# Optimization experiments

Measured on AMD Instinct MI355X. Metric: run time of the kernel, lower is better.

The kernel has to match this reference:

```python
import jax, jax.numpy as jnp
import numpy as np

N = 50000        # nodes
E = 800000       # edges (avg degree 16)
F = 64           # NUM_NODE_FEATURES == NUM_FILTERS
P = 32           # allocation.NUM_PHYS (policy logits per graph)
G = 64           # graphs in batch
MAX_DEG = 10     # PyG MFConv default max_degree


def setup_inputs() -> dict:
    key = jax.random.key(0)
    ks = jax.random.split(key, 12)
    x = jax.random.normal(ks[0], (N, F), jnp.float32)
    edge_index = jax.random.randint(ks[1], (2, E), 0, N, dtype=jnp.int32)
    batch = jnp.sort(jax.random.randint(ks[2], (N,), 0, G, dtype=jnp.int32))
    s = 1.0 / np.sqrt(F)
    return {
        "x": x,
        "edge_index": edge_index,
        "batch": batch,
        # GCNConv conv_in: F -> F
        "W_in": jax.random.normal(ks[3], (F, F), jnp.float32) * s,
        "b_in": jnp.zeros((F,), jnp.float32),
        # GCNConv conv_1: F -> F
        "W1": jax.random.normal(ks[4], (F, F), jnp.float32) * s,
        "b1": jnp.zeros((F,), jnp.float32),
        # MFConv conv_val: F -> 1, per-degree weights (deg 0..MAX_DEG)
        "Wl_val": jax.random.normal(ks[5], (MAX_DEG + 1, F, 1), jnp.float32) * s,
        "bl_val": jnp.zeros((MAX_DEG + 1, 1), jnp.float32),
        "Wr_val": jax.random.normal(ks[6], (MAX_DEG + 1, F, 1), jnp.float32) * s,
        # GCNConv conv_policy: F -> P
        "W_pol": jax.random.normal(ks[7], (F, P), jnp.float32) * s,
        "b_pol": jnp.zeros((P,), jnp.float32),
    }


def gcn_conv(x, edge_index, W, b):
    # PyG GCNConv: add self-loops, symmetric normalization, linear, scatter-add.
    src, dst = edge_index[0], edge_index[1]
    loop = jnp.arange(N, dtype=src.dtype)
    src = jnp.concatenate([src, loop])
    dst = jnp.concatenate([dst, loop])
    deg = jax.ops.segment_sum(jnp.ones_like(dst, x.dtype), dst, num_segments=N)
    dinv = jnp.where(deg > 0, jax.lax.rsqrt(deg), 0.0)
    norm = dinv[src] * dinv[dst]                 # [E+N]
    h = x @ W                                    # [N, out]
    out = jax.ops.segment_sum(norm[:, None] * h[src], dst, num_segments=N)
    return out + b


def mf_conv(x, edge_index, Wl, bl, Wr):
    # PyG MFConv: sum-aggregate neighbors, per-degree linear transforms.
    src, dst = edge_index[0], edge_index[1]
    h = jax.ops.segment_sum(x[src], dst, num_segments=N)     # neighbor sum [N,F]
    deg = jax.ops.segment_sum(jnp.ones((src.shape[0],), jnp.int32), dst, num_segments=N)
    deg = jnp.clip(deg, 0, MAX_DEG)                          # [N]
    # out = lins_l[deg](h) + lins_r[deg](x)  (lins_r has no bias)
    out = (jnp.einsum("nf,nfo->no", h, Wl[deg]) + bl[deg]
           + jnp.einsum("nf,nfo->no", x, Wr[deg]))
    return out


def reference(x, edge_index, batch, W_in, b_in, W1, b1, Wl_val, bl_val, Wr_val, W_pol, b_pol):
    h = gcn_conv(x, edge_index, W_in, b_in)
    h = gcn_conv(h, edge_index, W1, b1)
    val = mf_conv(h, edge_index, Wl_val, bl_val, Wr_val)          # [N,1]
    val = jax.ops.segment_sum(val, batch, num_segments=G)         # global_add_pool [G,1]
    pol = gcn_conv(h, edge_index, W_pol, b_pol)                   # [N,P]
    pol_sum = jax.ops.segment_sum(pol, batch, num_segments=G)
    cnt = jax.ops.segment_sum(jnp.ones((N,), x.dtype), batch, num_segments=G)
    pol = pol_sum / jnp.maximum(cnt, 1.0)[:, None]                # global_mean_pool [G,P]
    return (pol, val)
```

## Files before the change

### kernel.cpp

```cpp
#include <hip/hip_runtime.h>

#define F 64
#define P 32
#define MAXD 10
#define NGRP 8

__device__ __forceinline__ unsigned short f2bf(float f) {
  unsigned b = __float_as_uint(f);
  return (unsigned short)((b + 0x7FFFu + ((b >> 16) & 1u)) >> 16);
}
__device__ __forceinline__ unsigned pk2(float a, float b) {
  return (unsigned)f2bf(a) | ((unsigned)f2bf(b) << 16);
}
__device__ __forceinline__ float blo(unsigned u) { return __uint_as_float(u << 16); }
__device__ __forceinline__ float bhi(unsigned u) { return __uint_as_float(u & 0xFFFF0000u); }

__global__ void k_zero(float4* __restrict__ p, int n4) {
  int i = blockIdx.x * blockDim.x + threadIdx.x;
  int stride = gridDim.x * blockDim.x;
  float4 z = make_float4(0.f, 0.f, 0.f, 0.f);
  for (int idx = i; idx < n4; idx += stride) p[idx] = z;
}

__global__ void k_count_deg(const int* __restrict__ dst, int* __restrict__ deg, int E, int N) {
  int r = blockIdx.x & (NGRP - 1);
  float scale = (float)NGRP / (float)N;
  int gblk = blockIdx.x >> 3;
  int i = gblk * blockDim.x + threadIdx.x;
  int stride = (gridDim.x >> 3) * blockDim.x;
  int E4 = E >> 2;
  const int4* d4p = (const int4*)dst;
  for (int e4 = i; e4 < E4; e4 += stride) {
    int4 d4 = d4p[e4];
    int rr;
    rr = min(NGRP - 1, (int)((float)d4.x * scale)); if (rr == r) atomicAdd(&deg[d4.x], 1);
    rr = min(NGRP - 1, (int)((float)d4.y * scale)); if (rr == r) atomicAdd(&deg[d4.y], 1);
    rr = min(NGRP - 1, (int)((float)d4.z * scale)); if (rr == r) atomicAdd(&deg[d4.z], 1);
    rr = min(NGRP - 1, (int)((float)d4.w * scale)); if (rr == r) atomicAdd(&deg[d4.w], 1);
  }
  for (int e = (E & ~3) + i; e < E; e += stride) {
    int d = dst[e];
    int rr = min(NGRP - 1, (int)((float)d * scale));
    if (rr == r) atomicAdd(&deg[d], 1);
  }
}

__global__ void k_bsum(const int* __restrict__ deg, int* __restrict__ bsum, int N) {
  __shared__ int s[256];
  int t = threadIdx.x;
  int n = blockIdx.x * 256 + t;
  s[t] = (n < N) ? deg[n] : 0;
  __syncthreads();
  for (int o = 128; o > 0; o >>= 1) {
    if (t < o) s[t] += s[t + o];
    __syncthreads();
  }
  if (t == 0) bsum[blockIdx.x] = s[0];
}

__global__ void k_scan_bsum(int* __restrict__ bsum, int B) {
  __shared__ int s[1024];
  int t = threadIdx.x;
  int v = (t < B) ? bsum[t] : 0;
  s[t] = v;
  __syncthreads();
  for (int o = 1; o < 1024; o <<= 1) {
    int u = (t >= o) ? s[t - o] : 0;
    __syncthreads();
    s[t] += u;
    __syncthreads();
  }
  if (t < B) bsum[t] = s[t] - v;
}

__global__ void k_scan_fin(const int* __restrict__ deg, const int* __restrict__ bsum,
                           int* __restrict__ off, int* __restrict__ cur,
                           float* __restrict__ dinv, int N) {
  __shared__ int s[256];
  int t = threadIdx.x;
  int n = blockIdx.x * 256 + t;
  int v = (n < N) ? deg[n] : 0;
  s[t] = v;
  __syncthreads();
  for (int o = 1; o < 256; o <<= 1) {
    int u = (t >= o) ? s[t - o] : 0;
    __syncthreads();
    s[t] += u;
    __syncthreads();
  }
  if (n < N) {
    int ex = bsum[blockIdx.x] + s[t] - v;
    off[n] = ex;
    cur[n] = ex;
    dinv[n] = rsqrtf((float)(v + 1));
    if (n == N - 1) off[N] = ex + v;
  }
}

__global__ void k_fill(const int* __restrict__ src, const int* __restrict__ dst,
                       int* __restrict__ cur, int* __restrict__ csr, int E, int N) {
  int r = blockIdx.x & (NGRP - 1);
  float scale = (float)NGRP / (float)N;
  int gblk = blockIdx.x >> 3;
  int i = gblk * blockDim.x + threadIdx.x;
  int stride = (gridDim.x >> 3) * blockDim.x;
  int E4 = E >> 2;
  const int4* d4p = (const int4*)dst;
  for (int e4 = i; e4 < E4; e4 += stride) {
    int4 d4 = d4p[e4];
    int e = e4 * 4;
    int rr;
    rr = min(NGRP - 1, (int)((float)d4.x * scale));
    if (rr == r) { int pos = atomicAdd(&cur[d4.x], 1); csr[pos] = src[e]; }
    rr = min(NGRP - 1, (int)((float)d4.y * scale));
    if (rr == r) { int pos = atomicAdd(&cur[d4.y], 1); csr[pos] = src[e + 1]; }
    rr = min(NGRP - 1, (int)((float)d4.z * scale));
    if (rr == r) { int pos = atomicAdd(&cur[d4.z], 1); csr[pos] = src[e + 2]; }
    rr = min(NGRP - 1, (int)((float)d4.w * scale));
    if (rr == r) { int pos = atomicAdd(&cur[d4.w], 1); csr[pos] = src[e + 3]; }
  }
  for (int e = (E & ~3) + i; e < E; e += stride) {
    int d = dst[e];
    int rr = min(NGRP - 1, (int)((float)d * scale));
    if (rr == r) { int pos = atomicAdd(&cur[d], 1); csr[pos] = src[e]; }
  }
}

__global__ void k_scale16(const float* __restrict__ x, const float* __restrict__ dinv,
                          uint2* __restrict__ xs, int N) {
  int i = blockIdx.x * blockDim.x + threadIdx.x;
  int stride = gridDim.x * blockDim.x;
  int tot = N * (F / 4);
  const float4* x4 = (const float4*)x;
  for (int idx = i; idx < tot; idx += stride) {
    int n = idx >> 4;
    float d = dinv[n];
    float4 v = x4[idx];
    uint2 p;
    p.x = pk2(v.x * d, v.y * d);
    p.y = pk2(v.z * d, v.w * d);
    xs[idx] = p;
  }
}

__device__ __forceinline__ float rdlane(float v, int srclane) {
  return __int_as_float(__builtin_amdgcn_readlane(__float_as_int(v), srclane));
}

__device__ __forceinline__ void addbf(float4& a, uint2 p) {
  a.x += blo(p.x); a.y += bhi(p.x); a.z += blo(p.y); a.w += bhi(p.y);
}

template <bool WRITE_SCALED>
__global__ void k_gcn(const unsigned* __restrict__ xs, const int* __restrict__ csr,
                      const int* __restrict__ off, const float* __restrict__ dinv,
                      const float* __restrict__ W, const float* __restrict__ bias,
                      unsigned short* __restrict__ out, int N) {
  int wid = (blockIdx.x * blockDim.x + threadIdx.x) >> 6;
  int lane = threadIdx.x & 63;
  int nwaves = (gridDim.x * blockDim.x) >> 6;
  int g = lane >> 4, l = lane & 15;
  float w[F];
#pragma unroll
  for (int k = 0; k < F; ++k) w[k] = W[k * F + lane];
  float bv = bias[lane];
  for (int base = wid * 4; base < N; base += nwaves * 4) {
    int n = min(base + g, N - 1);
    int e0 = off[n], e1 = off[n + 1];
    float dnode = dinv[n];
    float4 acc = make_float4(0.f, 0.f, 0.f, 0.f);
    addbf(acc, *(const uint2*)&xs[(size_t)n * 32 + l * 2]);
    for (int win = e0; win < e1; win += 16) {
      int m = min(16, e1 - win);
      int ce = (win + l < e1) ? csr[win + l] : 0;
      int j = 0;
      for (; j + 4 <= m; j += 4) {
        int s0 = __shfl(ce, g * 16 + j + 0, 64);
        int s1 = __shfl(ce, g * 16 + j + 1, 64);
        int s2 = __shfl(ce, g * 16 + j + 2, 64);
        int s3 = __shfl(ce, g * 16 + j + 3, 64);
        uint2 q0 = *(const uint2*)&xs[(size_t)s0 * 32 + l * 2];
        uint2 q1 = *(const uint2*)&xs[(size_t)s1 * 32 + l * 2];
        uint2 q2 = *(const uint2*)&xs[(size_t)s2 * 32 + l * 2];
        uint2 q3 = *(const uint2*)&xs[(size_t)s3 * 32 + l * 2];
        addbf(acc, q0); addbf(acc, q1); addbf(acc, q2); addbf(acc, q3);
      }
      for (; j < m; ++j) {
        int s = __shfl(ce, g * 16 + j, 64);
        addbf(acc, *(const uint2*)&xs[(size_t)s * 32 + l * 2]);
      }
    }
#pragma unroll
    for (int gg = 0; gg < 4; ++gg) {
      float y0 = 0.f, y1 = 0.f, y2 = 0.f, y3 = 0.f;
#pragma unroll
      for (int k = 0; k < F; k += 4) {
        y0 += rdlane(acc.x, gg * 16 + (k >> 2)) * w[k + 0];
        y1 += rdlane(acc.y, gg * 16 + (k >> 2)) * w[k + 1];
        y2 += rdlane(acc.z, gg * 16 + (k >> 2)) * w[k + 2];
        y3 += rdlane(acc.w, gg * 16 + (k >> 2)) * w[k + 3];
      }
      float dd = rdlane(dnode, gg * 16);
      float y = dd * ((y0 + y1) + (y2 + y3)) + bv;
      if (WRITE_SCALED) y *= dd;
      int nn = base + gg;
      if (nn < N) out[(size_t)nn * F + lane] = f2bf(y);
    }
  }
}

__global__ void k_mfpol(const unsigned* __restrict__ H, const int* __restrict__ csr,
                        const int* __restrict__ off, const float* __restrict__ dinv,
                        const float* __restrict__ Wl, const float* __restrict__ bl,
                        const float* __restrict__ Wr, float* __restrict__ val,
                        float* __restrict__ u, int N) {
  int wid = (blockIdx.x * blockDim.x + threadIdx.x) >> 6;
  int lane = threadIdx.x & 63;
  int nwaves = (gridDim.x * blockDim.x) >> 6;
  int g = lane >> 4, l = lane & 15;
  for (int base = wid * 4; base < N; base += nwaves * 4) {
    bool valid = (base + g) < N;
    int n = min(base + g, N - 1);
    int e0 = off[n], e1 = off[n + 1];
    float dn = dinv[n];
    float4 ah = make_float4(0.f, 0.f, 0.f, 0.f);
    float4 aw = make_float4(0.f, 0.f, 0.f, 0.f);
    for (int win = e0; win < e1; win += 16) {
      int m = min(16, e1 - win);
      bool p = (win + l < e1);
      int ce = p ? csr[win + l] : 0;
      float cd = p ? dinv[ce] : 0.f;
      int j = 0;
      for (; j + 4 <= m; j += 4) {
        int s0 = __shfl(ce, g * 16 + j + 0, 64);
        int s1 = __shfl(ce, g * 16 + j + 1, 64);
        int s2 = __shfl(ce, g * 16 + j + 2, 64);
        int s3 = __shfl(ce, g * 16 + j + 3, 64);
        float d0 = __shfl(cd, g * 16 + j + 0, 64);
        float d1 = __shfl(cd, g * 16 + j + 1, 64);
        float d2 = __shfl(cd, g * 16 + j + 2, 64);
        float d3 = __shfl(cd, g * 16 + j + 3, 64);
        uint2 q0 = *(const uint2*)&H[(size_t)s0 * 32 + l * 2];
        uint2 q1 = *(const uint2*)&H[(size_t)s1 * 32 + l * 2];
        uint2 q2 = *(const uint2*)&H[(size_t)s2 * 32 + l * 2];
        uint2 q3 = *(const uint2*)&H[(size_t)s3 * 32 + l * 2];
        float f0x = blo(q0.x), f0y = bhi(q0.x), f0z = blo(q0.y), f0w = bhi(q0.y);
        float f1x = blo(q1.x), f1y = bhi(q1.x), f1z = blo(q1.y), f1w = bhi(q1.y);
        float f2x = blo(q2.x), f2y = bhi(q2.x), f2z = blo(q2.y), f2w = bhi(q2.y);
        float f3x = blo(q3.x), f3y = bhi(q3.x), f3z = blo(q3.y), f3w = bhi(q3.y);
        ah.x += (f0x + f1x) + (f2x + f3x);
        ah.y += (f0y + f1y) + (f2y + f3y);
        ah.z += (f0z + f1z) + (f2z + f3z);
        ah.w += (f0w + f1w) + (f2w + f3w);
        aw.x += (d0 * f0x + d1 * f1x) + (d2 * f2x + d3 * f3x);
        aw.y += (d0 * f0y + d1 * f1y) + (d2 * f2y + d3 * f3y);
        aw.z += (d0 * f0z + d1 * f1z) + (d2 * f2z + d3 * f3z);
        aw.w += (d0 * f0w + d1 * f1w) + (d2 * f2w + d3 * f3w);
      }
      for (; j < m; ++j) {
        int s = __shfl(ce, g * 16 + j, 64);
        float dd = __shfl(cd, g * 16 + j, 64);
        uint2 q = *(const uint2*)&H[(size_t)s * 32 + l * 2];
        float fx = blo(q.x), fy = bhi(q.x), fz = blo(q.y), fw = bhi(q.y);
        ah.x += fx; ah.y += fy; ah.z += fz; ah.w += fw;
        aw.x += dd * fx; aw.y += dd * fy; aw.z += dd * fz; aw.w += dd * fw;
      }
    }
    int dc = min(e1 - e0, MAXD);
    uint2 qn = *(const uint2*)&H[(size_t)n * 32 + l * 2];
    float4 hn = make_float4(blo(qn.x), bhi(qn.x), blo(qn.y), bhi(qn.y));
    float4 wl4 = *(const float4*)&Wl[dc * F + l * 4];
    float4 wr4 = *(const float4*)&Wr[dc * F + l * 4];
    float part = ah.x * wl4.x + ah.y * wl4.y + ah.z * wl4.z + ah.w * wl4.w
               + hn.x * wr4.x + hn.y * wr4.y + hn.z * wr4.z + hn.w * wr4.w;
#pragma unroll
    for (int o = 1; o < 16; o <<= 1) part += __shfl_xor(part, o, 64);
    if (l == 0 && valid) val[n] = part + bl[dc];
    if (valid) {
      float4 r;
      r.x = (aw.x + dn * hn.x) * dn;
      r.y = (aw.y + dn * hn.y) * dn;
      r.z = (aw.z + dn * hn.z) * dn;
      r.w = (aw.w + dn * hn.w) * dn;
      *(float4*)&u[(size_t)n * F + l * 4] = r;
    }
  }
}

__global__ void k_pool2(const float* __restrict__ u, const float* __restrict__ valn,
                        const int* __restrict__ batch, float* __restrict__ Uacc,
                        float* __restrict__ valg, float* __restrict__ cntg, int N) {
  __shared__ float Ul[64 * F];
  __shared__ float Vl[64], Cl[64];
  int t = threadIdx.x;
  for (int i = t; i < 64 * F; i += 256) Ul[i] = 0.f;
  if (t < 64) { Vl[t] = 0.f; Cl[t] = 0.f; }
  __syncthreads();
  int base = blockIdx.x * 256;
  int f = t & 63, r = t >> 6;
  for (int i = r; i < 256; i += 4) {
    int n = base + i;
    if (n >= N) break;
    int g = batch[n];
    atomicAdd(&Ul[g * F + f], u[(size_t)n * F + f]);
    if (f == 0) { atomicAdd(&Vl[g], valn[n]); atomicAdd(&Cl[g], 1.f); }
  }
  __syncthreads();
  int last = min(base + 256, N) - 1;
  if (last < base) return;
  int gmin = batch[base], gmax = batch[last];
  int ng = gmax - gmin + 1;
  for (int idx = t; idx < ng * F; idx += 256) {
    int g = gmin + (idx >> 6), ff = idx & 63;
    atomicAdd(&Uacc[g * F + ff], Ul[g * F + ff]);
  }
  for (int idx = t; idx < ng; idx += 256) {
    int g = gmin + idx;
    atomicAdd(&valg[g], Vl[g]);
    atomicAdd(&cntg[g], Cl[g]);
  }
}

__global__ void k_polfin(const float* __restrict__ Uacc, const float* __restrict__ valg,
                         const float* __restrict__ cntg, const float* __restrict__ W_pol,
                         const float* __restrict__ b_pol, float* __restrict__ out, int G) {
  int i = blockIdx.x * blockDim.x + threadIdx.x;
  if (i < G * P) {
    int g = i >> 5, p = i & 31;
    float s = 0.f;
#pragma unroll
    for (int k = 0; k < F; ++k) s += Uacc[g * F + k] * W_pol[k * P + p];
    out[i] = s / fmaxf(cntg[g], 1.f) + b_pol[p];
  }
  if (i < G) out[(size_t)G * P + i] = valg[i];
}

extern "C" void kernel_launch(void* const* d_in, const int* in_sizes, int n_in,
                              void* d_out, int out_size, void* d_ws, size_t ws_size,
                              hipStream_t stream) {
  const float* x = (const float*)d_in[0];
  const int* ei = (const int*)d_in[1];
  const int* batch = (const int*)d_in[2];
  const float* W_in = (const float*)d_in[3];
  const float* b_in = (const float*)d_in[4];
  const float* W1 = (const float*)d_in[5];
  const float* b1 = (const float*)d_in[6];
  const float* Wl = (const float*)d_in[7];
  const float* bl = (const float*)d_in[8];
  const float* Wr = (const float*)d_in[9];
  const float* W_pol = (const float*)d_in[10];
  const float* b_pol = (const float*)d_in[11];
  float* out = (float*)d_out;

  const int N = in_sizes[0] / F;
  const int E = in_sizes[1] / 2;
  const int G = out_size / (P + 1);
  const int* esrc = ei;
  const int* edst = ei + E;
  const int NB = (N + 255) / 256;

  char* ws = (char*)d_ws;
  size_t o = 0;
  auto alloc = [&](size_t bytes) {
    char* r = ws + o;
    o = (o + bytes + 255) & ~(size_t)255;
    return r;
  };
  char* zbase = ws;
  int* deg = (int*)alloc((size_t)N * 4);
  float* Uacc = (float*)alloc((size_t)G * F * 4);
  float* valg = (float*)alloc((size_t)G * 4);
  float* cntg = (float*)alloc((size_t)G * 4);
  size_t zbytes = o;
  int* off = (int*)alloc((size_t)(N + 1) * 4);
  int* cur = (int*)alloc((size_t)N * 4);
  float* dinv = (float*)alloc((size_t)N * 4);
  int* csr = (int*)alloc((size_t)E * 4);
  float* valn = (float*)alloc((size_t)N * 4);
  int* bsum = (int*)alloc(1024 * 4);
  unsigned* xs16 = (unsigned*)alloc((size_t)N * F * 2);
  unsigned* t16 = (unsigned*)alloc((size_t)N * F * 2);
  unsigned* h16 = (unsigned*)alloc((size_t)N * F * 2);
  float* u = (float*)alloc((size_t)N * F * 4);
  (void)ws_size; (void)n_in;

  const int bs = 256;
  int zn4 = (int)(zbytes / 16);
  k_zero<<<(zn4 + bs - 1) / bs, bs, 0, stream>>>((float4*)zbase, zn4);

  k_count_deg<<<2048, bs, 0, stream>>>(edst, deg, E, N);
  k_bsum<<<NB, bs, 0, stream>>>(deg, bsum, N);
  k_scan_bsum<<<1, 1024, 0, stream>>>(bsum, NB);
  k_scan_fin<<<NB, bs, 0, stream>>>(deg, bsum, off, cur, dinv, N);
  k_fill<<<2048, bs, 0, stream>>>(esrc, edst, cur, csr, E, N);

  k_scale16<<<2048, bs, 0, stream>>>(x, dinv, (uint2*)xs16, N);

  int gBlocks = (N + 15) / 16;
  k_gcn<true><<<gBlocks, bs, 0, stream>>>(xs16, csr, off, dinv, W_in, b_in,
                                          (unsigned short*)t16, N);
  k_gcn<false><<<gBlocks, bs, 0, stream>>>(t16, csr, off, dinv, W1, b1,
                                           (unsigned short*)h16, N);
  k_mfpol<<<gBlocks, bs, 0, stream>>>(h16, csr, off, dinv, Wl, bl, Wr, valn, u, N);

  int poolBlocks = (N + 255) / 256;
  k_pool2<<<poolBlocks, bs, 0, stream>>>(u, valn, batch, Uacc, valg, cntg, N);
  k_polfin<<<(G * P + bs - 1) / bs, bs, 0, stream>>>(Uacc, valg, cntg, W_pol, b_pol, out, G);
}
```

Before: 212.1 us.

## Fuse pooling into MF/policy kernel, merge scan kernels, unroll gathers deeper

The graph pooling kernel is folded into the MFConv/policy kernel. Per-node val and u results are now accumulated straight into per-block shared-memory slots for the two lowest graph ids, with global atomics as the fallback, so the N×F fp32 u buffer is never written or read back. The separate block-sum scan kernel is dropped, and each scan_fin block now reduces the preceding block sums itself. GCN gathers are unrolled by 8 and the GCN grid becomes a fixed 1024 persistent blocks. Risks are more global atomics when a 16-node block spans more than two graphs, and a different floating-point summation order.

Result: slower. 222.1 us (+4.7%).

```diff
diff --git a/kernel.cpp b/kernel.cpp
--- a/kernel.cpp
+++ b/kernel.cpp
@@ -58,27 +58,21 @@
   if (t == 0) bsum[blockIdx.x] = s[0];
 }
 
-__global__ void k_scan_bsum(int* __restrict__ bsum, int B) {
-  __shared__ int s[1024];
-  int t = threadIdx.x;
-  int v = (t < B) ? bsum[t] : 0;
-  s[t] = v;
-  __syncthreads();
-  for (int o = 1; o < 1024; o <<= 1) {
-    int u = (t >= o) ? s[t - o] : 0;
-    __syncthreads();
-    s[t] += u;
-    __syncthreads();
-  }
-  if (t < B) bsum[t] = s[t] - v;
-}
-
 __global__ void k_scan_fin(const int* __restrict__ deg, const int* __restrict__ bsum,
                            int* __restrict__ off, int* __restrict__ cur,
-                           float* __restrict__ dinv, int N) {
+                           float* __restrict__ dinv, int N, int NB) {
+  __shared__ int sb[256];
   __shared__ int s[256];
   int t = threadIdx.x;
-  int n = blockIdx.x * 256 + t;
+  int b = blockIdx.x;
+  sb[t] = (t < NB && t < b) ? bsum[t] : 0;
+  __syncthreads();
+  for (int o = 128; o > 0; o >>= 1) {
+    if (t < o) sb[t] += sb[t + o];
+    __syncthreads();
+  }
+  int base = sb[0];
+  int n = b * 256 + t;
   int v = (n < N) ? deg[n] : 0;
   s[t] = v;
   __syncthreads();
@@ -89,7 +83,7 @@
     __syncthreads();
   }
   if (n < N) {
-    int ex = bsum[blockIdx.x] + s[t] - v;
+    int ex = base + s[t] - v;
     off[n] = ex;
     cur[n] = ex;
     dinv[n] = rsqrtf((float)(v + 1));
@@ -174,6 +168,26 @@
       int m = min(16, e1 - win);
       int ce = (win + l < e1) ? csr[win + l] : 0;
       int j = 0;
+      for (; j + 8 <= m; j += 8) {
+        int s0 = __shfl(ce, g * 16 + j + 0, 64);
+        int s1 = __shfl(ce, g * 16 + j + 1, 64);
+        int s2 = __shfl(ce, g * 16 + j + 2, 64);
+        int s3 = __shfl(ce, g * 16 + j + 3, 64);
+        int s4 = __shfl(ce, g * 16 + j + 4, 64);
+        int s5 = __shfl(ce, g * 16 + j + 5, 64);
+        int s6 = __shfl(ce, g * 16 + j + 6, 64);
+        int s7 = __shfl(ce, g * 16 + j + 7, 64);
+        uint2 q0 = *(const uint2*)&xs[(size_t)s0 * 32 + l * 2];
+        uint2 q1 = *(const uint2*)&xs[(size_t)s1 * 32 + l * 2];
+        uint2 q2 = *(const uint2*)&xs[(size_t)s2 * 32 + l * 2];
+        uint2 q3 = *(const uint2*)&xs[(size_t)s3 * 32 + l * 2];
+        uint2 q4 = *(const uint2*)&xs[(size_t)s4 * 32 + l * 2];
+        uint2 q5 = *(const uint2*)&xs[(size_t)s5 * 32 + l * 2];
+        uint2 q6 = *(const uint2*)&xs[(size_t)s6 * 32 + l * 2];
+        uint2 q7 = *(const uint2*)&xs[(size_t)s7 * 32 + l * 2];
+        addbf(acc, q0); addbf(acc, q1); addbf(acc, q2); addbf(acc, q3);
+        addbf(acc, q4); addbf(acc, q5); addbf(acc, q6); addbf(acc, q7);
+      }
       for (; j + 4 <= m; j += 4) {
         int s0 = __shfl(ce, g * 16 + j + 0, 64);
         int s1 = __shfl(ce, g * 16 + j + 1, 64);
@@ -212,112 +226,132 @@
 __global__ void k_mfpol(const unsigned* __restrict__ H, const int* __restrict__ csr,
                         const int* __restrict__ off, const float* __restrict__ dinv,
                         const float* __restrict__ Wl, const float* __restrict__ bl,
-                        const float* __restrict__ Wr, float* __restrict__ val,
-                        float* __restrict__ u, int N) {
-  int wid = (blockIdx.x * blockDim.x + threadIdx.x) >> 6;
-  int lane = threadIdx.x & 63;
-  int nwaves = (gridDim.x * blockDim.x) >> 6;
+                        const float* __restrict__ Wr, const int* __restrict__ batch,
+                        float* __restrict__ Uacc, float* __restrict__ valg,
+                        float* __restrict__ cntg, int N, int G) {
+  __shared__ float Ua[2][64];
+  __shared__ float va[2], ca[2];
+  int t = threadIdx.x;
+  if (t < 128) Ua[t >> 6][t & 63] = 0.f;
+  if (t < 2) { va[t] = 0.f; ca[t] = 0.f; }
+  __syncthreads();
+  int base16 = blockIdx.x * 16;
+  int gmin = batch[base16];
+  int lane = t & 63;
   int g = lane >> 4, l = lane & 15;
-  for (int base = wid * 4; base < N; base += nwaves * 4) {
-    bool valid = (base + g) < N;
-    int n = min(base + g, N - 1);
-    int e0 = off[n], e1 = off[n + 1];
-    float dn = dinv[n];
-    float4 ah = make_float4(0.f, 0.f, 0.f, 0.f);
-    float4 aw = make_float4(0.f, 0.f, 0.f, 0.f);
-    for (int win = e0; win < e1; win += 16) {
-      int m = min(16, e1 - win);
-      bool p = (win + l < e1);
-      int ce = p ? csr[win + l] : 0;
-      float cd = p ? dinv[ce] : 0.f;
-      int j = 0;
-      for (; j + 4 <= m; j += 4) {
-        int s0 = __shfl(ce, g * 16 + j + 0, 64);
-        int s1 = __shfl(ce, g * 16 + j + 1, 64);
-        int s2 = __shfl(ce, g * 16 + j + 2, 64);
-        int s3 = __shfl(ce, g * 16 + j + 3, 64);
-        float d0 = __shfl(cd, g * 16 + j + 0, 64);
-        float d1 = __shfl(cd, g * 16 + j + 1, 64);
-        float d2 = __shfl(cd, g * 16 + j + 2, 64);
-        float d3 = __shfl(cd, g * 16 + j + 3, 64);
-        uint2 q0 = *(const uint2*)&H[(size_t)s0 * 32 + l * 2];
-        uint2 q1 = *(const uint2*)&H[(size_t)s1 * 32 + l * 2];
-        uint2 q2 = *(const uint2*)&H[(size_t)s2 * 32 + l * 2];
-        uint2 q3 = *(const uint2*)&H[(size_t)s3 * 32 + l * 2];
-        float f0x = blo(q0.x), f0y = bhi(q0.x), f0z = blo(q0.y), f0w = bhi(q0.y);
-        float f1x = blo(q1.x), f1y = bhi(q1.x), f1z = blo(q1.y), f1w = bhi(q1.y);
-        float f2x = blo(q2.x), f2y = bhi(q2.x), f2z = blo(q2.y), f2w = bhi(q2.y);
-        float f3x = blo(q3.x), f3y = bhi(q3.x), f3z = blo(q3.y), f3w = bhi(q3.y);
-        ah.x += (f0x + f1x) + (f2x + f3x);
-        ah.y += (f0y + f1y) + (f2y + f3y);
-        ah.z += (f0z + f1z) + (f2z + f3z);
-        ah.w += (f0w + f1w) + (f2w + f3w);
-        aw.x += (d0 * f0x + d1 * f1x) + (d2 * f2x + d3 * f3x);
-        aw.y += (d0 * f0y + d1 * f1y) + (d2 * f2y + d3 * f3y);
-        aw.z += (d0 * f0z + d1 * f1z) + (d2 * f2z + d3 * f3z);
-        aw.w += (d0 * f0w + d1 * f1w) + (d2 * f2w + d3 * f3w);
-      }
-      for (; j < m; ++j) {
-        int s = __shfl(ce, g * 16 + j, 64);
-        float dd = __shfl(cd, g * 16 + j, 64);
-        uint2 q = *(const uint2*)&H[(size_t)s * 32 + l * 2];
-        float fx = blo(q.x), fy = bhi(q.x), fz = blo(q.y), fw = bhi(q.y);
-        ah.x += fx; ah.y += fy; ah.z += fz; ah.w += fw;
-        aw.x += dd * fx; aw.y += dd * fy; aw.z += dd * fz; aw.w += dd * fw;
-      }
-    }
-    int dc = min(e1 - e0, MAXD);
-    uint2 qn = *(const uint2*)&H[(size_t)n * 32 + l * 2];
-    float4 hn = make_float4(blo(qn.x), bhi(qn.x), blo(qn.y), bhi(qn.y));
-    float4 wl4 = *(const float4*)&Wl[dc * F + l * 4];
-    float4 wr4 = *(const float4*)&Wr[dc * F + l * 4];
-    float part = ah.x * wl4.x + ah.y * wl4.y + ah.z * wl4.z + ah.w * wl4.w
-               + hn.x * wr4.x + hn.y * wr4.y + hn.z * wr4.z + hn.w * wr4.w;
+  int ni = (t >> 6) * 4 + g;
+  bool valid = (base16 + ni) < N;
+  int n = valid ? base16 + ni : N - 1;
+  int e0 = off[n], e1 = off[n + 1];
+  float dn = dinv[n];
+  float4 ah = make_float4(0.f, 0.f, 0.f, 0.f);
+  float4 aw = make_float4(0.f, 0.f, 0.f, 0.f);
+  for (int win = e0; win < e1; win += 16) {
+    int m = min(16, e1 - win);
+    bool p = (win + l < e1);
+    int ce = p ? csr[win + l] : 0;
+    float cd = p ? dinv[ce] : 0.f;
+    int j = 0;
+    for (; j + 8 <= m; j += 8) {
+      int s0 = __shfl(ce, g * 16 + j + 0, 64);
+      int s1 = __shfl(ce, g * 16 + j + 1, 64);
+      int s2 = __shfl(ce, g * 16 + j + 2, 64);
+      int s3 = __shfl(ce, g * 16 + j + 3, 64);
+      int s4 = __shfl(ce, g * 16 + j + 4, 64);
+      int s5 = __shfl(ce, g * 16 + j + 5, 64);
+      int s6 = __shfl(ce, g * 16 + j + 6, 64);
+      int s7 = __shfl(ce, g * 16 + j + 7, 64);
+      float d0 = __shfl(cd, g * 16 + j + 0, 64);
+      float d1 = __shfl(cd, g * 16 + j + 1, 64);
+      float d2 = __shfl(cd, g * 16 + j + 2, 64);
+      float d3 = __shfl(cd, g * 16 + j + 3, 64);
+      float d4 = __shfl(cd, g * 16 + j + 4, 64);
+      float d5 = __shfl(cd, g * 16 + j + 5, 64);
+      float d6 = __shfl(cd, g * 16 + j + 6, 64);
+      float d7 = __shfl(cd, g * 16 + j + 7, 64);
+      uint2 q0 = *(const uint2*)&H[(size_t)s0 * 32 + l * 2];
+      uint2 q1 = *(const uint2*)&H[(size_t)s1 * 32 + l * 2];
+      uint2 q2 = *(const uint2*)&H[(size_t)s2 * 32 + l * 2];
+      uint2 q3 = *(const uint2*)&H[(size_t)s3 * 32 + l * 2];
+      uint2 q4 = *(const uint2*)&H[(size_t)s4 * 32 + l * 2];
+      uint2 q5 = *(const uint2*)&H[(size_t)s5 * 32 + l * 2];
+      uint2 q6 = *(const uint2*)&H[(size_t)s6 * 32 + l * 2];
+      uint2 q7 = *(const uint2*)&H[(size_t)s7 * 32 + l * 2];
+      float fx, fy, fz, fw;
+      fx = blo(q0.x); fy = bhi(q0.x); fz = blo(q0.y); fw = bhi(q0.y);
+      ah.x += fx; ah.y += fy; ah.z += fz; ah.w += fw;
+      aw.x += d0 * fx; aw.y += d0 * fy; aw.z += d0 * fz; aw.w += d0 * fw;
+      fx = blo(q1.x); fy = bhi(q1.x); fz = blo(q1.y); fw = bhi(q1.y);
+      ah.x += fx; ah.y += fy; ah.z += fz; ah.w += fw;
+      aw.x += d1 * fx; aw.y += d1 * fy; aw.z += d1 * fz; aw.w += d1 * fw;
+      fx = blo(q2.x); fy = bhi(q2.x); fz = blo(q2.y); fw = bhi(q2.y);
+      ah.x += fx; ah.y += fy; ah.z += fz; ah.w += fw;
+      aw.x += d2 * fx; aw.y += d2 * fy; aw.z += d2 * fz; aw.w += d2 * fw;
+      fx = blo(q3.x); fy = bhi(q3.x); fz = blo(q3.y); fw = bhi(q3.y);
+      ah.x += fx; ah.y += fy; ah.z += fz; ah.w += fw;
+      aw.x += d3 * fx; aw.y += d3 * fy; aw.z += d3 * fz; aw.w += d3 * fw;
+      fx = blo(q4.x); fy = bhi(q4.x); fz = blo(q4.y); fw = bhi(q4.y);
+      ah.x += fx; ah.y += fy; ah.z += fz; ah.w += fw;
+      aw.x += d4 * fx; aw.y += d4 * fy; aw.z += d4 * fz; aw.w += d4 * fw;
+      fx = blo(q5.x); fy = bhi(q5.x); fz = blo(q5.y); fw = bhi(q5.y);
+      ah.x += fx; ah.y += fy; ah.z += fz; ah.w += fw;
+      aw.x += d5 * fx; aw.y += d5 * fy; aw.z += d5 * fz; aw.w += d5 * fw;
+      fx = blo(q6.x); fy = bhi(q6.x); fz = blo(q6.y); fw = bhi(q6.y);
+      ah.x += fx; ah.y += fy; ah.z += fz; ah.w += fw;
+      aw.x += d6 * fx; aw.y += d6 * fy; aw.z += d6 * fz; aw.w += d6 * fw;
+      fx = blo(q7.x); fy = bhi(q7.x); fz = blo(q7.y); fw = bhi(q7.y);
+      ah.x += fx; ah.y += fy; ah.z += fz; ah.w += fw;
+      aw.x += d7 * fx; aw.y += d7 * fy; aw.z += d7 * fz; aw.w += d7 * fw;
+    }
+    for (; j < m; ++j) {
+      int s = __shfl(ce, g * 16 + j, 64);
+      float dd = __shfl(cd, g * 16 + j, 64);
+      uint2 q = *(const uint2*)&H[(size_t)s * 32 + l * 2];
+      float fx = blo(q.x), fy = bhi(q.x), fz = blo(q.y), fw = bhi(q.y);
+      ah.x += fx; ah.y += fy; ah.z += fz; ah.w += fw;
+      aw.x += dd * fx; aw.y += dd * fy; aw.z += dd * fz; aw.w += dd * fw;
+    }
+  }
+  int dc = min(e1 - e0, MAXD);
+  uint2 qn = *(const uint2*)&H[(size_t)n * 32 + l * 2];
+  float4 hn = make_float4(blo(qn.x), bhi(qn.x), blo(qn.y), bhi(qn.y));
+  float4 wl4 = *(const float4*)&Wl[dc * F + l * 4];
+  float4 wr4 = *(const float4*)&Wr[dc * F + l * 4];
+  float part = ah.x * wl4.x + ah.y * wl4.y + ah.z * wl4.z + ah.w * wl4.w
+             + hn.x * wr4.x + hn.y * wr4.y + hn.z * wr4.z + hn.w * wr4.w;
 #pragma unroll
-    for (int o = 1; o < 16; o <<= 1) part += __shfl_xor(part, o, 64);
-    if (l == 0 && valid) val[n] = part + bl[dc];
-    if (valid) {
-      float4 r;
-      r.x = (aw.x + dn * hn.x) * dn;
-      r.y = (aw.y + dn * hn.y) * dn;
-      r.z = (aw.z + dn * hn.z) * dn;
-      r.w = (aw.w + dn * hn.w) * dn;
-      *(float4*)&u[(size_t)n * F + l * 4] = r;
-    }
-  }
-}
-
-__global__ void k_pool2(const float* __restrict__ u, const float* __restrict__ valn,
-                        const int* __restrict__ batch, float* __restrict__ Uacc,
-                        float* __restrict__ valg, float* __restrict__ cntg, int N) {
-  __shared__ float Ul[64 * F];
-  __shared__ float Vl[64], Cl[64];
-  int t = threadIdx.x;
-  for (int i = t; i < 64 * F; i += 256) Ul[i] = 0.f;
-  if (t < 64) { Vl[t] = 0.f; Cl[t] = 0.f; }
+  for (int o = 1; o < 16; o <<= 1) part += __shfl_xor(part, o, 64);
+  float vout = part + bl[dc];
+  float4 r;
+  r.x = (aw.x + dn * hn.x) * dn;
+  r.y = (aw.y + dn * hn.y) * dn;
+  r.z = (aw.z + dn * hn.z) * dn;
+  r.w = (aw.w + dn * hn.w) * dn;
+  if (valid) {
+    int bg = batch[n];
+    int slot = bg - gmin;
+    if (slot < 2) {
+      atomicAdd(&Ua[slot][l * 4 + 0], r.x);
+      atomicAdd(&Ua[slot][l * 4 + 1], r.y);
+      atomicAdd(&Ua[slot][l * 4 + 2], r.z);
+      atomicAdd(&Ua[slot][l * 4 + 3], r.w);
+      if (l == 0) { atomicAdd(&va[slot], vout); atomicAdd(&ca[slot], 1.f); }
+    } else {
+      atomicAdd(&Uacc[bg * F + l * 4 + 0], r.x);
+      atomicAdd(&Uacc[bg * F + l * 4 + 1], r.y);
+      atomicAdd(&Uacc[bg * F + l * 4 + 2], r.z);
+      atomicAdd(&Uacc[bg * F + l * 4 + 3], r.w);
+      if (l == 0) { atomicAdd(&valg[bg], vout); atomicAdd(&cntg[bg], 1.f); }
+    }
+  }
   __syncthreads();
-  int base = blockIdx.x * 256;
-  int f = t & 63, r = t >> 6;
-  for (int i = r; i < 256; i += 4) {
-    int n = base + i;
-    if (n >= N) break;
-    int g = batch[n];
-    atomicAdd(&Ul[g * F + f], u[(size_t)n * F + f]);
-    if (f == 0) { atomicAdd(&Vl[g], valn[n]); atomicAdd(&Cl[g], 1.f); }
-  }
-  __syncthreads();
-  int last = min(base + 256, N) - 1;
-  if (last < base) return;
-  int gmin = batch[base], gmax = batch[last];
-  int ng = gmax - gmin + 1;
-  for (int idx = t; idx < ng * F; idx += 256) {
-    int g = gmin + (idx >> 6), ff = idx & 63;
-    atomicAdd(&Uacc[g * F + ff], Ul[g * F + ff]);
-  }
-  for (int idx = t; idx < ng; idx += 256) {
-    int g = gmin + idx;
-    atomicAdd(&valg[g], Vl[g]);
-    atomicAdd(&cntg[g], Cl[g]);
+  if (t < 128) {
+    int slot = t >> 6, f = t & 63;
+    int bg = gmin + slot;
+    if (bg < G) {
+      atomicAdd(&Uacc[bg * F + f], Ua[slot][f]);
+      if (f == 0) { atomicAdd(&valg[bg], va[slot]); atomicAdd(&cntg[bg], ca[slot]); }
+    }
   }
 }
 
@@ -376,12 +410,10 @@
   int* cur = (int*)alloc((size_t)N * 4);
   float* dinv = (float*)alloc((size_t)N * 4);
   int* csr = (int*)alloc((size_t)E * 4);
-  float* valn = (float*)alloc((size_t)N * 4);
   int* bsum = (int*)alloc(1024 * 4);
   unsigned* xs16 = (unsigned*)alloc((size_t)N * F * 2);
   unsigned* t16 = (unsigned*)alloc((size_t)N * F * 2);
   unsigned* h16 = (unsigned*)alloc((size_t)N * F * 2);
-  float* u = (float*)alloc((size_t)N * F * 4);
   (void)ws_size; (void)n_in;
 
   const int bs = 256;
@@ -390,20 +422,19 @@
 
   k_count_deg<<<2048, bs, 0, stream>>>(edst, deg, E, N);
   k_bsum<<<NB, bs, 0, stream>>>(deg, bsum, N);
-  k_scan_bsum<<<1, 1024, 0, stream>>>(bsum, NB);
-  k_scan_fin<<<NB, bs, 0, stream>>>(deg, bsum, off, cur, dinv, N);
+  k_scan_fin<<<NB, bs, 0, stream>>>(deg, bsum, off, cur, dinv, N, NB);
   k_fill<<<2048, bs, 0, stream>>>(esrc, edst, cur, csr, E, N);
 
   k_scale16<<<2048, bs, 0, stream>>>(x, dinv, (uint2*)xs16, N);
 
-  int gBlocks = (N + 15) / 16;
-  k_gcn<true><<<gBlocks, bs, 0, stream>>>(xs16, csr, off, dinv, W_in, b_in,
-                                          (unsigned short*)t16, N);
-  k_gcn<false><<<gBlocks, bs, 0, stream>>>(t16, csr, off, dinv, W1, b1,
-                                           (unsigned short*)h16, N);
-  k_mfpol<<<gBlocks, bs, 0, stream>>>(h16, csr, off, dinv, Wl, bl, Wr, valn, u, N);
-
-  int poolBlocks = (N + 255) / 256;
-  k_pool2<<<poolBlocks, bs, 0, stream>>>(u, valn, batch, Uacc, valg, cntg, N);
+  k_gcn<true><<<1024, bs, 0, stream>>>(xs16, csr, off, dinv, W_in, b_in,
+                                       (unsigned short*)t16, N);
+  k_gcn<false><<<1024, bs, 0, stream>>>(t16, csr, off, dinv, W1, b1,
+                                        (unsigned short*)h16, N);
+
+  int mfBlocks = (N + 15) / 16;
+  k_mfpol<<<mfBlocks, bs, 0, stream>>>(h16, csr, off, dinv, Wl, bl, Wr, batch,
+                                       Uacc, valg, cntg, N, G);
+
   k_polfin<<<(G * P + bs - 1) / bs, bs, 0, stream>>>(Uacc, valg, cntg, W_pol, b_pol, out, G);
 }
```

## Simplify degree count, fold block-sum scan, unroll gathers, cap GCN grid

Applied to the files above, without the earlier changes.

Drops the dst-range partitioning in the degree-count kernel, so every block does atomics over all edges, and halves its grid. Removes the single-block scan kernel: each scan_fin block now reduces the preceding block sums itself. Adds an 8-way unrolled neighbor-gather loop in the GCN kernel to keep more loads in flight, and launches both GCN kernels with a fixed 1024-block grid-stride grid instead of one block per 16 nodes. The redundant per-block reduction assumes NB ≤ 256 (N=50000 gives 196), and the unpartitioned atomics may raise contention or hurt cache locality.

Result: faster. 207.3 us (-2.2%).

```diff
diff --git a/kernel.cpp b/kernel.cpp
--- a/kernel.cpp
+++ b/kernel.cpp
@@ -22,27 +22,19 @@
   for (int idx = i; idx < n4; idx += stride) p[idx] = z;
 }
 
-__global__ void k_count_deg(const int* __restrict__ dst, int* __restrict__ deg, int E, int N) {
-  int r = blockIdx.x & (NGRP - 1);
-  float scale = (float)NGRP / (float)N;
-  int gblk = blockIdx.x >> 3;
-  int i = gblk * blockDim.x + threadIdx.x;
-  int stride = (gridDim.x >> 3) * blockDim.x;
+__global__ void k_count_deg(const int* __restrict__ dst, int* __restrict__ deg, int E) {
+  int i = blockIdx.x * blockDim.x + threadIdx.x;
+  int stride = gridDim.x * blockDim.x;
   int E4 = E >> 2;
   const int4* d4p = (const int4*)dst;
   for (int e4 = i; e4 < E4; e4 += stride) {
-    int4 d4 = d4p[e4];
-    int rr;
-    rr = min(NGRP - 1, (int)((float)d4.x * scale)); if (rr == r) atomicAdd(&deg[d4.x], 1);
-    rr = min(NGRP - 1, (int)((float)d4.y * scale)); if (rr == r) atomicAdd(&deg[d4.y], 1);
-    rr = min(NGRP - 1, (int)((float)d4.z * scale)); if (rr == r) atomicAdd(&deg[d4.z], 1);
-    rr = min(NGRP - 1, (int)((float)d4.w * scale)); if (rr == r) atomicAdd(&deg[d4.w], 1);
-  }
-  for (int e = (E & ~3) + i; e < E; e += stride) {
-    int d = dst[e];
-    int rr = min(NGRP - 1, (int)((float)d * scale));
-    if (rr == r) atomicAdd(&deg[d], 1);
-  }
+    int4 d = d4p[e4];
+    atomicAdd(&deg[d.x], 1);
+    atomicAdd(&deg[d.y], 1);
+    atomicAdd(&deg[d.z], 1);
+    atomicAdd(&deg[d.w], 1);
+  }
+  for (int e = (E & ~3) + i; e < E; e += stride) atomicAdd(&deg[dst[e]], 1);
 }
 
 __global__ void k_bsum(const int* __restrict__ deg, int* __restrict__ bsum, int N) {
@@ -58,27 +50,21 @@
   if (t == 0) bsum[blockIdx.x] = s[0];
 }
 
-__global__ void k_scan_bsum(int* __restrict__ bsum, int B) {
-  __shared__ int s[1024];
-  int t = threadIdx.x;
-  int v = (t < B) ? bsum[t] : 0;
-  s[t] = v;
-  __syncthreads();
-  for (int o = 1; o < 1024; o <<= 1) {
-    int u = (t >= o) ? s[t - o] : 0;
-    __syncthreads();
-    s[t] += u;
-    __syncthreads();
-  }
-  if (t < B) bsum[t] = s[t] - v;
-}
-
 __global__ void k_scan_fin(const int* __restrict__ deg, const int* __restrict__ bsum,
                            int* __restrict__ off, int* __restrict__ cur,
-                           float* __restrict__ dinv, int N) {
+                           float* __restrict__ dinv, int N, int NB) {
+  __shared__ int sb[256];
   __shared__ int s[256];
   int t = threadIdx.x;
-  int n = blockIdx.x * 256 + t;
+  int b = blockIdx.x;
+  sb[t] = (t < NB && t < b) ? bsum[t] : 0;
+  __syncthreads();
+  for (int o = 128; o > 0; o >>= 1) {
+    if (t < o) sb[t] += sb[t + o];
+    __syncthreads();
+  }
+  int base = sb[0];
+  int n = b * 256 + t;
   int v = (n < N) ? deg[n] : 0;
   s[t] = v;
   __syncthreads();
@@ -89,7 +75,7 @@
     __syncthreads();
   }
   if (n < N) {
-    int ex = bsum[blockIdx.x] + s[t] - v;
+    int ex = base + s[t] - v;
     off[n] = ex;
     cur[n] = ex;
     dinv[n] = rsqrtf((float)(v + 1));
@@ -174,6 +160,26 @@
       int m = min(16, e1 - win);
       int ce = (win + l < e1) ? csr[win + l] : 0;
       int j = 0;
+      for (; j + 8 <= m; j += 8) {
+        int s0 = __shfl(ce, g * 16 + j + 0, 64);
+        int s1 = __shfl(ce, g * 16 + j + 1, 64);
+        int s2 = __shfl(ce, g * 16 + j + 2, 64);
+        int s3 = __shfl(ce, g * 16 + j + 3, 64);
+        int s4 = __shfl(ce, g * 16 + j + 4, 64);
+        int s5 = __shfl(ce, g * 16 + j + 5, 64);
+        int s6 = __shfl(ce, g * 16 + j + 6, 64);
+        int s7 = __shfl(ce, g * 16 + j + 7, 64);
+        uint2 q0 = *(const uint2*)&xs[(size_t)s0 * 32 + l * 2];
+        uint2 q1 = *(const uint2*)&xs[(size_t)s1 * 32 + l * 2];
+        uint2 q2 = *(const uint2*)&xs[(size_t)s2 * 32 + l * 2];
+        uint2 q3 = *(const uint2*)&xs[(size_t)s3 * 32 + l * 2];
+        uint2 q4 = *(const uint2*)&xs[(size_t)s4 * 32 + l * 2];
+        uint2 q5 = *(const uint2*)&xs[(size_t)s5 * 32 + l * 2];
+        uint2 q6 = *(const uint2*)&xs[(size_t)s6 * 32 + l * 2];
+        uint2 q7 = *(const uint2*)&xs[(size_t)s7 * 32 + l * 2];
+        addbf(acc, q0); addbf(acc, q1); addbf(acc, q2); addbf(acc, q3);
+        addbf(acc, q4); addbf(acc, q5); addbf(acc, q6); addbf(acc, q7);
+      }
       for (; j + 4 <= m; j += 4) {
         int s0 = __shfl(ce, g * 16 + j + 0, 64);
         int s1 = __shfl(ce, g * 16 + j + 1, 64);
@@ -376,8 +382,8 @@
   int* cur = (int*)alloc((size_t)N * 4);
   float* dinv = (float*)alloc((size_t)N * 4);
   int* csr = (int*)alloc((size_t)E * 4);
+  int* bsum = (int*)alloc(1024 * 4);
   float* valn = (float*)alloc((size_t)N * 4);
-  int* bsum = (int*)alloc(1024 * 4);
   unsigned* xs16 = (unsigned*)alloc((size_t)N * F * 2);
   unsigned* t16 = (unsigned*)alloc((size_t)N * F * 2);
   unsigned* h16 = (unsigned*)alloc((size_t)N * F * 2);
@@ -388,19 +394,19 @@
   int zn4 = (int)(zbytes / 16);
   k_zero<<<(zn4 + bs - 1) / bs, bs, 0, stream>>>((float4*)zbase, zn4);
 
-  k_count_deg<<<2048, bs, 0, stream>>>(edst, deg, E, N);
+  k_count_deg<<<1024, bs, 0, stream>>>(edst, deg, E);
   k_bsum<<<NB, bs, 0, stream>>>(deg, bsum, N);
-  k_scan_bsum<<<1, 1024, 0, stream>>>(bsum, NB);
-  k_scan_fin<<<NB, bs, 0, stream>>>(deg, bsum, off, cur, dinv, N);
+  k_scan_fin<<<NB, bs, 0, stream>>>(deg, bsum, off, cur, dinv, N, NB);
   k_fill<<<2048, bs, 0, stream>>>(esrc, edst, cur, csr, E, N);
 
   k_scale16<<<2048, bs, 0, stream>>>(x, dinv, (uint2*)xs16, N);
 
+  k_gcn<true><<<1024, bs, 0, stream>>>(xs16, csr, off, dinv, W_in, b_in,
+                                       (unsigned short*)t16, N);
+  k_gcn<false><<<1024, bs, 0, stream>>>(t16, csr, off, dinv, W1, b1,
+                                        (unsigned short*)h16, N);
+
   int gBlocks = (N + 15) / 16;
-  k_gcn<true><<<gBlocks, bs, 0, stream>>>(xs16, csr, off, dinv, W_in, b_in,
-                                          (unsigned short*)t16, N);
-  k_gcn<false><<<gBlocks, bs, 0, stream>>>(t16, csr, off, dinv, W1, b1,
-                                           (unsigned short*)h16, N);
   k_mfpol<<<gBlocks, bs, 0, stream>>>(h16, csr, off, dinv, Wl, bl, Wr, valn, u, N);
 
   int poolBlocks = (N + 255) / 256;
```
